# Kernel tuning notes

Measured on AMD Instinct MI355X. Metric: run time of the kernel, lower is better.

The kernel has to match this reference:

```python
import jax, jax.numpy as jnp
import numpy as np

HEADS = 16
DIMS = [64, 64, 64, 64]  # [d_att(Q), d_att(K), d_ff(V), d_ff(G)]
EPS = 1e-4
P_POW = 2


def _cdist(Q, K):
    # Euclidean pairwise distance via the norm expansion, like torch.cdist.
    # Q: [h, b, t, d], K: [h, b, t, d] -> [h, b, t, t]
    q2 = jnp.sum(Q * Q, axis=-1)  # [h, b, t]
    k2 = jnp.sum(K * K, axis=-1)  # [h, b, t]
    qk = jnp.einsum('hbtd,hbsd->hbts', Q, K)
    d2 = q2[..., :, None] + k2[..., None, :] - 2.0 * qk
    return jnp.sqrt(jnp.maximum(d2, 0.0))


def setup_inputs() -> dict:
    key = jax.random.key(0)
    ks = jax.random.split(key, 4)
    b, t, d_in = 2, 2048, 1024
    d_proj = HEADS * sum(DIMS)  # 4096
    X = jax.random.normal(ks[0], (b, t, d_in), dtype=jnp.float32)
    W_in = jax.random.normal(ks[1], (d_in, d_proj), dtype=jnp.float32) * (d_in ** -0.5)
    b_in = jnp.zeros((d_proj,), dtype=jnp.float32)
    W_out = jax.random.normal(ks[2], (HEADS * DIMS[2], d_in), dtype=jnp.float32) * ((HEADS * DIMS[2]) ** -0.5)
    b_out = jnp.zeros((d_in,), dtype=jnp.float32)
    return {"X": X, "W_in": W_in, "b_in": b_in, "W_out": W_out, "b_out": b_out}


def reference(X, W_in, b_in, W_out, b_out):
    b, t, _ = X.shape
    # multi-head input projection: [b,t,d_in] -> [h,b,t,sum(DIMS)] -> split
    P = X @ W_in + b_in                       # [b, t, h*sum(DIMS)]
    P = P.reshape(b, t, HEADS, sum(DIMS))
    P = jnp.transpose(P, (2, 0, 1, 3))        # [h, b, t, sum(DIMS)]
    splits = np.cumsum(DIMS)[:-1]
    Q, K, V, G = jnp.split(P, splits, axis=-1)
    # Shepard's attention: inverse-power-distance weights
    W = jnp.power(EPS + _cdist(Q, K), -P_POW)         # [h, b, t, t]
    W = W / (EPS + jnp.sum(W, axis=-1, keepdims=True))
    A = jnp.einsum('hbts,hbse->hbte', W, V)           # [h, b, t, e]
    H = G * A                                          # gating
    H = jnp.transpose(H, (1, 2, 0, 3)).reshape(b, t, HEADS * DIMS[2])
    return H @ W_out + b_out
```

## Files before the change

### kernel.cpp

```cpp
#include <hip/hip_runtime.h>
#include <hip/hip_bf16.h>
#include <cstdint>
#include <cstddef>

typedef __bf16 bf16_t;
typedef __attribute__((ext_vector_type(8))) __bf16 bf16x8;
typedef __attribute__((ext_vector_type(4))) float f32x4;
typedef __attribute__((ext_vector_type(16))) float f32x16;
typedef __attribute__((ext_vector_type(4))) unsigned int u32x4;

#define ATT_EPS 1e-4f

__device__ __forceinline__ f32x4 mfma_bf16(bf16x8 a, bf16x8 b, f32x4 c) {
  return __builtin_amdgcn_mfma_f32_16x16x32_bf16(a, b, c, 0, 0, 0);
}
__device__ __forceinline__ f32x16 mfma32(bf16x8 a, bf16x8 b, f32x16 c) {
  return __builtin_amdgcn_mfma_f32_32x32x16_bf16(a, b, c, 0, 0, 0);
}
__device__ __forceinline__ unsigned cvtpk_bf16(float lo, float hi) {
  unsigned r;
  asm("v_cvt_pk_bf16_f32 %0, %1, %2" : "=v"(r) : "v"(lo), "v"(hi));
  return r;
}

#define GLDS16(g, l)                                                          \
  __builtin_amdgcn_global_load_lds(                                           \
      (const __attribute__((address_space(1))) void*)(g),                     \
      (__attribute__((address_space(3))) void*)(l), 16, 0, 0)

#define BARRAW() asm volatile("s_barrier" ::: "memory")
#define WAITV4() asm volatile("s_waitcnt vmcnt(4)" ::: "memory")
#define WAITV0() asm volatile("s_waitcnt vmcnt(0)" ::: "memory")

__global__ __launch_bounds__(256) void cvt_x_kernel(
    const float* __restrict__ X, bf16_t* __restrict__ Xb, int n8) {
  int i = blockIdx.x * 256 + threadIdx.x;
  if (i >= n8) return;
  f32x4 a = ((const f32x4*)X)[i * 2 + 0];
  f32x4 b = ((const f32x4*)X)[i * 2 + 1];
  bf16x8 o;
  o[0] = (__bf16)a[0]; o[1] = (__bf16)a[1]; o[2] = (__bf16)a[2]; o[3] = (__bf16)a[3];
  o[4] = (__bf16)b[0]; o[5] = (__bf16)b[1]; o[6] = (__bf16)b[2]; o[7] = (__bf16)b[3];
  ((bf16x8*)Xb)[i] = o;
}

__global__ __launch_bounds__(256) void tcvt2_kernel(
    const float* __restrict__ Wi, bf16_t* __restrict__ WiT,
    const float* __restrict__ Wo, bf16_t* __restrict__ WoT) {
  __shared__ float T[64][65];
  int tx = threadIdx.x & 63, ty = threadIdx.x >> 6;
  const float* W;
  bf16_t* Wt;
  int c0, r0, R, C;
  if (blockIdx.y < 16) {
    W = Wi; Wt = WiT; R = 1024; C = 4096;
    c0 = blockIdx.x * 64; r0 = blockIdx.y * 64;
  } else {
    int idx = (blockIdx.y - 16) * 64 + blockIdx.x;
    if (idx >= 256) return;
    W = Wo; Wt = WoT; R = 1024; C = 1024;
    c0 = (idx & 15) * 64; r0 = (idx >> 4) * 64;
  }
#pragma unroll
  for (int i = 0; i < 16; ++i) {
    int rr = ty * 16 + i;
    T[rr][tx] = W[(size_t)(r0 + rr) * C + c0 + tx];
  }
  __syncthreads();
#pragma unroll
  for (int i = 0; i < 16; ++i) {
    int cc = ty * 16 + i;
    Wt[(size_t)(c0 + cc) * R + r0 + tx] = (bf16_t)T[tx][cc];
  }
}

__global__ __launch_bounds__(512, 2) void gemm1_kernel(
    const bf16_t* __restrict__ A, const bf16_t* __restrict__ Bt,
    const float* __restrict__ bias, bf16_t* __restrict__ P,
    float* __restrict__ Q2, bf16_t* __restrict__ K2E, bf16_t* __restrict__ VtG) {
  __shared__ bf16_t As[4][2][128 * 32];
  __shared__ bf16_t Bs[4][2][128 * 32];

  const int K = 1024, N = 4096;
  int tid = threadIdx.x, lane = tid & 63, wv = tid >> 6;
  int l15 = lane & 15, lhi = lane >> 4;
  int wm = wv >> 2, wn = wv & 3;
  int swz = (blockIdx.x & 7) * 32 + (blockIdx.x >> 3);
  int tm = swz >> 4, tn = swz & 15;
  int m0 = tm << 8, n0 = tn << 8;
  int h = tn;

  int srow = tid >> 2, su = tid & 3;
  int scc = (su ^ ((srow >> 1) & 3)) << 3;
  auto stage2 = [&](int t, int pq) {
    int k0 = t * 32 + scc;
    if (pq == 0) {
      GLDS16(A + (size_t)(m0 + srow) * K + k0, &As[t & 3][0][tid * 8]);
      GLDS16(A + (size_t)(m0 + 128 + srow) * K + k0, &As[t & 3][1][tid * 8]);
    } else {
      GLDS16(Bt + (size_t)(n0 + srow) * K + k0, &Bs[t & 3][0][tid * 8]);
      GLDS16(Bt + (size_t)(n0 + 128 + srow) * K + k0, &Bs[t & 3][1][tid * 8]);
    }
  };

  f32x4 zero = {0.f, 0.f, 0.f, 0.f};
  f32x4 acc[8][4];
#pragma unroll
  for (int mf = 0; mf < 8; ++mf)
#pragma unroll
    for (int nf = 0; nf < 4; ++nf) acc[mf][nf] = zero;

  int bh = wn >> 1;
  int cidb = (wn & 1) * 64 + l15;

  stage2(0, 0); stage2(0, 1);
  stage2(1, 0); stage2(1, 1);
  WAITV4();
  BARRAW();

  for (int t = 0; t < 32; ++t) {
    int buf = t & 3;
    bf16x8 af0[4], bfr[4];
#pragma unroll
    for (int i = 0; i < 4; ++i) {
      int mfr = i * 16 + l15;
      af0[i] = *(const bf16x8*)&As[buf][wm][mfr * 32 + ((lhi ^ ((mfr >> 1) & 3)) << 3)];
    }
#pragma unroll
    for (int nf = 0; nf < 4; ++nf) {
      int cid = cidb + nf * 16;
      bfr[nf] = *(const bf16x8*)&Bs[buf][bh][cid * 32 + ((lhi ^ ((cid >> 1) & 3)) << 3)];
    }
    if (t + 2 < 32) stage2(t + 2, 0);
#pragma unroll
    for (int i = 0; i < 4; ++i)
#pragma unroll
      for (int nf = 0; nf < 4; ++nf)
        acc[i][nf] = mfma_bf16(af0[i], bfr[nf], acc[i][nf]);
    bf16x8 af1[4];
#pragma unroll
    for (int i = 0; i < 4; ++i) {
      int mfr = (4 + i) * 16 + l15;
      af1[i] = *(const bf16x8*)&As[buf][wm][mfr * 32 + ((lhi ^ ((mfr >> 1) & 3)) << 3)];
    }
    if (t + 2 < 32) stage2(t + 2, 1);
#pragma unroll
    for (int i = 0; i < 4; ++i)
#pragma unroll
      for (int nf = 0; nf < 4; ++nf)
        acc[4 + i][nf] = mfma_bf16(af1[i], bfr[nf], acc[4 + i][nf]);
    if (t < 30) WAITV4();
    else if (t == 30) WAITV0();
    BARRAW();
  }

#pragma unroll
  for (int nf = 0; nf < 4; ++nf) {
    float bv = bias[n0 + wn * 64 + nf * 16 + l15];
#pragma unroll
    for (int mf = 0; mf < 8; ++mf)
#pragma unroll
      for (int r = 0; r < 4; ++r) acc[mf][nf][r] += bv;
  }

  if (wn != 2) {
#pragma unroll
    for (int nf = 0; nf < 4; ++nf) {
      int col = n0 + wn * 64 + nf * 16 + l15;
#pragma unroll
      for (int mf = 0; mf < 8; ++mf) {
        int rowb = m0 + wm * 128 + mf * 16 + lhi * 4;
#pragma unroll
        for (int r = 0; r < 4; ++r)
          P[(size_t)(rowb + r) * N + col] = (bf16_t)acc[mf][nf][r];
      }
    }
  }

  if (wn < 2) {
#pragma unroll
    for (int mf = 0; mf < 8; ++mf)
#pragma unroll
      for (int r = 0; r < 4; ++r) {
        float s = 0.f;
#pragma unroll
        for (int nf = 0; nf < 4; ++nf) s += acc[mf][nf][r] * acc[mf][nf][r];
        s += __shfl_xor(s, 1);
        s += __shfl_xor(s, 2);
        s += __shfl_xor(s, 4);
        s += __shfl_xor(s, 8);
        if (l15 == 0) {
          int row = m0 + wm * 128 + mf * 16 + lhi * 4 + r;
          if (wn == 0) {
            Q2[h * 4096 + row] = s;
          } else {
            __bf16 kh = (__bf16)s;
            __bf16 kl = (__bf16)(s - (float)kh);
            bf16x8 rw;
            rw[0] = kh; rw[1] = kl;
            rw[2] = (__bf16)1.f; rw[3] = (__bf16)1.f;
            rw[4] = (__bf16)0.f; rw[5] = (__bf16)0.f;
            rw[6] = (__bf16)0.f; rw[7] = (__bf16)0.f;
            *(bf16x8*)&K2E[((size_t)h * 4096 + row) * 8] = rw;
          }
        }
      }
  }

  bf16_t* T = &As[0][0][0];
  if (wn == 2) {
#pragma unroll
    for (int mf = 0; mf < 8; ++mf)
#pragma unroll
      for (int nf = 0; nf < 4; ++nf)
#pragma unroll
        for (int r = 0; r < 4; ++r) {
          int row = wm * 128 + mf * 16 + lhi * 4 + r;
          int e = nf * 16 + l15;
          int prow = (row & ~15) | ((row & 3) | ((row & 4) << 1) | ((row & 8) >> 1));
          T[e * 264 + prow] = (bf16_t)acc[mf][nf][r];
        }
  }
  __syncthreads();
  {
    int e = tid >> 3, c0 = (tid & 7) * 32;
    bf16_t* dst = VtG + (size_t)(h * 64 + e) * 4096 + m0 + c0;
#pragma unroll
    for (int j = 0; j < 4; ++j)
      *(bf16x8*)&dst[j * 8] = *(bf16x8*)&T[e * 264 + c0 + j * 8];
  }
}

template <int OUTF32>
__global__ __launch_bounds__(256, 2) void gemm_kernel(
    const bf16_t* __restrict__ A, const bf16_t* __restrict__ Bt,
    const float* __restrict__ bias, void* __restrict__ Cout,
    int M, int N, int K) {
  __shared__ bf16_t As[2][128 * 64];
  __shared__ bf16_t Bs[2][128 * 64];
  int tid = threadIdx.x, lane = tid & 63, wv = tid >> 6;
  int l15 = lane & 15, lhi = lane >> 4;
  int NT = N >> 7;
  int nwg = gridDim.x;
  int qq = nwg >> 3;
  int swz = (blockIdx.x & 7) * qq + (blockIdx.x >> 3);
  int tm = swz / NT, tn = swz % NT;
  int m0 = tm << 7, n0 = tn << 7;
  int wm = (wv >> 1) << 6, wn = (wv & 1) << 6;
  int KT = K >> 6;

  auto stage = [&](int buf, int kt) {
    int k0 = kt << 6;
#pragma unroll
    for (int s = 0; s < 4; ++s) {
      int t = s * 256 + tid;
      int row = t >> 3, u = t & 7;
      int cc = (u ^ (row & 7)) << 3;
      GLDS16(A + (size_t)(m0 + row) * K + k0 + cc, &As[buf][t * 8]);
    }
#pragma unroll
    for (int s = 0; s < 4; ++s) {
      int t = s * 256 + tid;
      int row = t >> 3, u = t & 7;
      int cc = (u ^ (row & 7)) << 3;
      GLDS16(Bt + (size_t)(n0 + row) * K + k0 + cc, &Bs[buf][t * 8]);
    }
  };

  f32x4 zero = {0.f, 0.f, 0.f, 0.f};
  f32x4 acc[4][4];
#pragma unroll
  for (int ms = 0; ms < 4; ++ms)
#pragma unroll
    for (int ns = 0; ns < 4; ++ns) acc[ms][ns] = zero;

  stage(0, 0);
  __syncthreads();
  int cur = 0;
  for (int kt = 0; kt < KT; ++kt) {
    if (kt + 1 < KT) stage(cur ^ 1, kt + 1);
#pragma unroll
    for (int ks = 0; ks < 2; ++ks) {
      bf16x8 af[4], bfr[4];
#pragma unroll
      for (int ms = 0; ms < 4; ++ms) {
        int row = wm + ms * 16 + l15;
        af[ms] = *(const bf16x8*)&As[cur][row * 64 + (((ks * 4 + lhi) ^ (row & 7)) << 3)];
      }
#pragma unroll
      for (int ns = 0; ns < 4; ++ns) {
        int col = wn + ns * 16 + l15;
        bfr[ns] = *(const bf16x8*)&Bs[cur][col * 64 + (((ks * 4 + lhi) ^ (col & 7)) << 3)];
      }
#pragma unroll
      for (int ms = 0; ms < 4; ++ms)
#pragma unroll
        for (int ns = 0; ns < 4; ++ns)
          acc[ms][ns] = mfma_bf16(af[ms], bfr[ns], acc[ms][ns]);
    }
    __syncthreads();
    cur ^= 1;
  }

#pragma unroll
  for (int ns = 0; ns < 4; ++ns) {
    int col = n0 + wn + ns * 16 + l15;
    float bv = bias[col];
#pragma unroll
    for (int ms = 0; ms < 4; ++ms) {
      int rowb = m0 + wm + ms * 16 + lhi * 4;
#pragma unroll
      for (int r = 0; r < 4; ++r) {
        float v = acc[ms][ns][r] + bv;
        if (OUTF32)
          ((float*)Cout)[(size_t)(rowb + r) * N + col] = v;
        else
          ((bf16_t*)Cout)[(size_t)(rowb + r) * N + col] = (bf16_t)v;
      }
    }
  }
}

__global__ __launch_bounds__(512, 4) void attn_kernel(
    const bf16_t* __restrict__ P, const bf16_t* __restrict__ VtG,
    const float* __restrict__ Q2, const bf16_t* __restrict__ K2E,
    bf16_t* __restrict__ H) {
  __shared__ union Smem {
    struct {
      bf16_t Ks[2][64 * 64];
      bf16_t Vts[2][64 * 64];
      bf16_t K2e[2][64 * 8];
    } l;
    float Comb[4][64][33];
  } sm;
  __shared__ float invLds[4][32];

  int tid = threadIdx.x, lane = tid & 63, wv = tid >> 6;
  int l31 = lane & 31, hi = lane >> 5, hi4 = hi * 4;
  int qw = wv & 3, sw = wv >> 2;
  int sOff = sw * 32;
  int swz = (blockIdx.x & 7) * 64 + (blockIdx.x >> 3);
  int hb = swz >> 4, qt = swz & 15;
  int h = hb >> 1, b = hb & 1;
  int rowbase = b * 2048;
  const bf16_t* Pq = P + (size_t)rowbase * 4096 + h * 256;
  const bf16_t* Pk = Pq + 64;
  const bf16_t* Pg = Pq + 192;
  const bf16_t* Vg = VtG + (size_t)h * 64 * 4096 + rowbase;
  const float* Q2g = Q2 + h * 4096 + rowbase;
  const bf16_t* K2Eg = K2E + ((size_t)h * 4096 + rowbase) * 8;
  int q0 = qt * 128 + qw * 32;

  auto stageKV = [&](int buf, int s0) {
    {
      int row = tid >> 3, u = tid & 7;
      int cc = (u ^ (row & 7)) << 3;
      GLDS16(Pk + (size_t)(s0 + row) * 4096 + cc, &sm.l.Ks[buf][tid * 8]);
    }
    {
      int row = tid >> 3, u = tid & 7;
      int cc = (u ^ (row & 7)) << 3;
      GLDS16(Vg + (size_t)row * 4096 + s0 + cc, &sm.l.Vts[buf][tid * 8]);
    }
    if (tid < 64)
      GLDS16(K2Eg + (size_t)(s0 + tid) * 8, &sm.l.K2e[buf][tid * 8]);
  };

  bf16x8 qm[4];
#pragma unroll
  for (int db = 0; db < 4; ++db) {
    bf16x8 q = *(const bf16x8*)(Pq + (size_t)(q0 + l31) * 4096 + db * 16 + hi * 8);
    u32x4 u = *(u32x4*)&q;
    u = (u ^ 0x80008000u) + 0x00800080u;
    qm[db] = *(bf16x8*)&u;
  }
  float q2s = Q2g[q0 + l31];
  __bf16 q2h = (__bf16)q2s;
  __bf16 q2l = (__bf16)(q2s - (float)q2h);
  bf16x8 qmE;
  qmE[0] = hi ? (__bf16)0.f : (__bf16)1.f;
  qmE[1] = qmE[0];
  qmE[2] = hi ? (__bf16)0.f : q2h;
  qmE[3] = hi ? (__bf16)0.f : q2l;
  qmE[4] = (__bf16)0.f; qmE[5] = (__bf16)0.f;
  qmE[6] = (__bf16)0.f; qmE[7] = (__bf16)0.f;

  f32x16 zero16;
#pragma unroll
  for (int r = 0; r < 16; ++r) zero16[r] = 0.f;

  f32x16 nacc0 = zero16, nacc1 = zero16;
  float dacc0 = 0.f, dacc1 = 0.f;

  stageKV(0, 0);
  __syncthreads();

  for (int st = 0; st < 32; ++st) {
    int cur = st & 1;
    int s0 = st * 64;
    if (st + 1 < 32) stageKV(cur ^ 1, s0 + 64);

    const bf16_t* KsC = sm.l.Ks[cur];
    const bf16_t* VtC = sm.l.Vts[cur];
    const bf16_t* K2eC = sm.l.K2e[cur];
    {
      int srow = sOff + l31;
      bf16x8 ke = *(const bf16x8*)&K2eC[srow * 8];
      u32x4 keu = *(u32x4*)&ke;
      u32x4 kz;
      kz[0] = hi ? 0u : keu[0];
      kz[1] = hi ? 0u : keu[1];
      kz[2] = 0u; kz[3] = 0u;
      bf16x8 kfE = *(bf16x8*)&kz;
      f32x16 D = mfma32(kfE, qmE, zero16);
#pragma unroll
      for (int db = 0; db < 4; ++db) {
        bf16x8 kf = *(const bf16x8*)&KsC[srow * 64 + (((db * 2 + hi) ^ (srow & 7)) << 3)];
        D = mfma32(kf, qm[db], D);
      }
      float p[16];
#pragma unroll
      for (int r = 0; r < 16; ++r) {
        float w = __builtin_amdgcn_rcpf(fmaxf(D[r], 1e-12f));
        if (r & 1) dacc1 += w; else dacc0 += w;
        p[r] = w;
      }
      u32x4 w0v = {cvtpk_bf16(p[0], p[1]), cvtpk_bf16(p[2], p[3]),
                   cvtpk_bf16(p[4], p[5]), cvtpk_bf16(p[6], p[7])};
      u32x4 w1v = {cvtpk_bf16(p[8], p[9]), cvtpk_bf16(p[10], p[11]),
                   cvtpk_bf16(p[12], p[13]), cvtpk_bf16(p[14], p[15])};
      bf16x8 pa0 = *(bf16x8*)&w0v;
      bf16x8 pa1 = *(bf16x8*)&w1v;
      int e = l31;
      int ciB = sw * 4;
      bf16x8 vb00 = *(const bf16x8*)&VtC[e * 64 + (((ciB + 0 + hi) ^ (e & 7)) << 3)];
      bf16x8 vb01 = *(const bf16x8*)&VtC[(e + 32) * 64 + (((ciB + 0 + hi) ^ ((e + 32) & 7)) << 3)];
      bf16x8 vb10 = *(const bf16x8*)&VtC[e * 64 + (((ciB + 2 + hi) ^ (e & 7)) << 3)];
      bf16x8 vb11 = *(const bf16x8*)&VtC[(e + 32) * 64 + (((ciB + 2 + hi) ^ ((e + 32) & 7)) << 3)];
      nacc0 = mfma32(pa0, vb00, nacc0);
      nacc1 = mfma32(pa0, vb01, nacc1);
      nacc0 = mfma32(pa1, vb10, nacc0);
      nacc1 = mfma32(pa1, vb11, nacc1);
    }
    __syncthreads();
  }

  if (sw == 1) {
#pragma unroll
    for (int r = 0; r < 16; ++r) {
      sm.Comb[qw][lane][r] = nacc0[r];
      sm.Comb[qw][lane][16 + r] = nacc1[r];
    }
    sm.Comb[qw][lane][32] = dacc0 + dacc1;
  }
  __syncthreads();
  if (sw == 0) {
    float dacc = dacc0 + dacc1 + sm.Comb[qw][lane][32];
#pragma unroll
    for (int r = 0; r < 16; ++r) {
      nacc0[r] += sm.Comb[qw][lane][r];
      nacc1[r] += sm.Comb[qw][lane][16 + r];
    }
    dacc += __shfl_xor(dacc, 32);
    float inv = __builtin_amdgcn_rcpf(ATT_EPS + dacc);
    if (lane < 32) invLds[qw][l31] = inv;
    __builtin_amdgcn_s_waitcnt(0);
#pragma unroll
    for (int r = 0; r < 16; ++r) {
      int q = (r & 3) + 8 * (r >> 2) + hi4;
      int tq = q0 + q;
      float iv = invLds[qw][q];
      float g0 = (float)Pg[(size_t)tq * 4096 + l31];
      float g1 = (float)Pg[(size_t)tq * 4096 + 32 + l31];
      H[(size_t)(rowbase + tq) * 1024 + h * 64 + l31] = (bf16_t)(g0 * nacc0[r] * iv);
      H[(size_t)(rowbase + tq) * 1024 + h * 64 + 32 + l31] = (bf16_t)(g1 * nacc1[r] * iv);
    }
  }
}

extern "C" void kernel_launch(void* const* d_in, const int* in_sizes, int n_in,
                              void* d_out, int out_size, void* d_ws, size_t ws_size,
                              hipStream_t stream) {
  const float* X     = (const float*)d_in[0];
  const float* W_in  = (const float*)d_in[1];
  const float* b_in  = (const float*)d_in[2];
  const float* W_out = (const float*)d_in[3];
  const float* b_out = (const float*)d_in[4];

  char* ws = (char*)d_ws;
  bf16_t* Xb  = (bf16_t*)(ws);
  bf16_t* WbT = (bf16_t*)(ws + ((size_t)8  << 20));
  bf16_t* WoT = (bf16_t*)(ws + ((size_t)16 << 20));
  bf16_t* Pb  = (bf16_t*)(ws + ((size_t)18 << 20));
  bf16_t* Hb  = (bf16_t*)(ws + ((size_t)50 << 20));
  float*  Q2  = (float*) (ws + ((size_t)58 << 20));
  bf16_t* VtG = (bf16_t*)d_out;
  bf16_t* K2E = (bf16_t*)((char*)d_out + ((size_t)8 << 20));

  cvt_x_kernel<<<2048, 256, 0, stream>>>(X, Xb, 4096 * 1024 / 8);
  tcvt2_kernel<<<dim3(64, 20), 256, 0, stream>>>(W_in, WbT, W_out, WoT);
  gemm1_kernel<<<256, 512, 0, stream>>>(Xb, WbT, b_in, Pb, Q2, K2E, VtG);
  attn_kernel<<<512, 512, 0, stream>>>(Pb, VtG, Q2, K2E, Hb);
  gemm_kernel<1><<<256, 256, 0, stream>>>(Hb, WoT, b_out, d_out, 4096, 1024, 1024);
}
```

Before: 130.1 us.

## Fuse X conversion into weight-transpose kernel and deepen gemm1 prefetch to three stages

The X fp32-to-bf16 conversion is merged into the weight transpose/convert kernel as extra grid rows, which removes one kernel launch. Each thread now converts 16 elements instead of 8. In gemm1, the global-to-LDS prefetch distance goes from 2 to 3 tiles using the existing 4-slot buffer, and the vmcnt waits are adjusted to match. The deeper prefetch is meant to hide more load latency, but it leaves less slack between a slot being refilled and the last reads from it, and it keeps more loads in flight.

```diff
diff --git a/kernel.cpp b/kernel.cpp
--- a/kernel.cpp
+++ b/kernel.cpp
@@ -29,25 +29,28 @@
       (__attribute__((address_space(3))) void*)(l), 16, 0, 0)
 
 #define BARRAW() asm volatile("s_barrier" ::: "memory")
+#define WAITV8() asm volatile("s_waitcnt vmcnt(8)" ::: "memory")
 #define WAITV4() asm volatile("s_waitcnt vmcnt(4)" ::: "memory")
 #define WAITV0() asm volatile("s_waitcnt vmcnt(0)" ::: "memory")
 
-__global__ __launch_bounds__(256) void cvt_x_kernel(
-    const float* __restrict__ X, bf16_t* __restrict__ Xb, int n8) {
-  int i = blockIdx.x * 256 + threadIdx.x;
-  if (i >= n8) return;
-  f32x4 a = ((const f32x4*)X)[i * 2 + 0];
-  f32x4 b = ((const f32x4*)X)[i * 2 + 1];
-  bf16x8 o;
-  o[0] = (__bf16)a[0]; o[1] = (__bf16)a[1]; o[2] = (__bf16)a[2]; o[3] = (__bf16)a[3];
-  o[4] = (__bf16)b[0]; o[5] = (__bf16)b[1]; o[6] = (__bf16)b[2]; o[7] = (__bf16)b[3];
-  ((bf16x8*)Xb)[i] = o;
-}
-
-__global__ __launch_bounds__(256) void tcvt2_kernel(
+__global__ __launch_bounds__(256) void prep_kernel(
     const float* __restrict__ Wi, bf16_t* __restrict__ WiT,
-    const float* __restrict__ Wo, bf16_t* __restrict__ WoT) {
+    const float* __restrict__ Wo, bf16_t* __restrict__ WoT,
+    const float* __restrict__ X, bf16_t* __restrict__ Xb) {
   __shared__ float T[64][65];
+  if (blockIdx.y >= 20) {
+    int i = ((blockIdx.y - 20) * 64 + blockIdx.x) * 256 + threadIdx.x;
+    const f32x4* src = (const f32x4*)X + (size_t)i * 4;
+    f32x4 a = src[0], b = src[1], c = src[2], d = src[3];
+    bf16x8 o0, o1;
+    o0[0] = (__bf16)a[0]; o0[1] = (__bf16)a[1]; o0[2] = (__bf16)a[2]; o0[3] = (__bf16)a[3];
+    o0[4] = (__bf16)b[0]; o0[5] = (__bf16)b[1]; o0[6] = (__bf16)b[2]; o0[7] = (__bf16)b[3];
+    o1[0] = (__bf16)c[0]; o1[1] = (__bf16)c[1]; o1[2] = (__bf16)c[2]; o1[3] = (__bf16)c[3];
+    o1[4] = (__bf16)d[0]; o1[5] = (__bf16)d[1]; o1[6] = (__bf16)d[2]; o1[7] = (__bf16)d[3];
+    ((bf16x8*)Xb)[(size_t)i * 2] = o0;
+    ((bf16x8*)Xb)[(size_t)i * 2 + 1] = o1;
+    return;
+  }
   int tx = threadIdx.x & 63, ty = threadIdx.x >> 6;
   const float* W;
   bf16_t* Wt;
@@ -115,7 +118,8 @@
 
   stage2(0, 0); stage2(0, 1);
   stage2(1, 0); stage2(1, 1);
-  WAITV4();
+  stage2(2, 0); stage2(2, 1);
+  WAITV8();
   BARRAW();
 
   for (int t = 0; t < 32; ++t) {
@@ -131,7 +135,7 @@
       int cid = cidb + nf * 16;
       bfr[nf] = *(const bf16x8*)&Bs[buf][bh][cid * 32 + ((lhi ^ ((cid >> 1) & 3)) << 3)];
     }
-    if (t + 2 < 32) stage2(t + 2, 0);
+    if (t + 3 < 32) stage2(t + 3, 0);
 #pragma unroll
     for (int i = 0; i < 4; ++i)
 #pragma unroll
@@ -143,13 +147,14 @@
       int mfr = (4 + i) * 16 + l15;
       af1[i] = *(const bf16x8*)&As[buf][wm][mfr * 32 + ((lhi ^ ((mfr >> 1) & 3)) << 3)];
     }
-    if (t + 2 < 32) stage2(t + 2, 1);
+    if (t + 3 < 32) stage2(t + 3, 1);
 #pragma unroll
     for (int i = 0; i < 4; ++i)
 #pragma unroll
       for (int nf = 0; nf < 4; ++nf)
         acc[4 + i][nf] = mfma_bf16(af1[i], bfr[nf], acc[4 + i][nf]);
-    if (t < 30) WAITV4();
+    if (t <= 28) WAITV8();
+    else if (t == 29) WAITV4();
     else if (t == 30) WAITV0();
     BARRAW();
   }
@@ -497,8 +502,7 @@
   bf16_t* VtG = (bf16_t*)d_out;
   bf16_t* K2E = (bf16_t*)((char*)d_out + ((size_t)8 << 20));
 
-  cvt_x_kernel<<<2048, 256, 0, stream>>>(X, Xb, 4096 * 1024 / 8);
-  tcvt2_kernel<<<dim3(64, 20), 256, 0, stream>>>(W_in, WbT, W_out, WoT);
+  prep_kernel<<<dim3(64, 36), 256, 0, stream>>>(W_in, WbT, W_out, WoT, X, Xb);
   gemm1_kernel<<<256, 512, 0, stream>>>(Xb, WbT, b_in, Pb, Q2, K2E, VtG);
   attn_kernel<<<512, 512, 0, stream>>>(Pb, VtG, Q2, K2E, Hb);
   gemm_kernel<1><<<256, 256, 0, stream>>>(Hb, WoT, b_out, d_out, 4096, 1024, 1024);
```

Result: faster. 127.4 us (-2.1%).
